# Optimization experiments

Measured on AMD Instinct MI355X. Metric: run time of the kernel, lower is better.

The kernel has to match this reference:

```python
import jax, jax.numpy as jnp
import numpy as np

GROUPS = 32
EPS = 1e-5


def setup_inputs() -> dict:
    key = jax.random.key(0)
    ks = jax.random.split(key, 8)
    B, C, H, W = 4, 512, 64, 64
    s = 1.0 / np.sqrt(C)  # conv1x1 fan-in init scale
    return {
        "x": jax.random.normal(ks[0], (B, C, H, W), dtype=jnp.float32),
        "gn_gamma": jnp.ones((C,), dtype=jnp.float32),
        "gn_beta": jnp.zeros((C,), dtype=jnp.float32),
        "wq": jax.random.normal(ks[1], (C, C), dtype=jnp.float32) * s,
        "bq": jnp.zeros((C,), dtype=jnp.float32),
        "wk": jax.random.normal(ks[2], (C, C), dtype=jnp.float32) * s,
        "bk": jnp.zeros((C,), dtype=jnp.float32),
        "wv": jax.random.normal(ks[3], (C, C), dtype=jnp.float32) * s,
        "bv": jnp.zeros((C,), dtype=jnp.float32),
    }


def reference(x, gn_gamma, gn_beta, wq, bq, wk, bk, wv, bv):
    B, C, H, W = x.shape
    N = H * W
    # GroupNorm over (channels-within-group, H, W)
    xg = x.reshape(B, GROUPS, C // GROUPS, H, W)
    mean = xg.mean(axis=(2, 3, 4), keepdims=True)
    var = xg.var(axis=(2, 3, 4), keepdims=True)
    xn = ((xg - mean) * jax.lax.rsqrt(var + EPS)).reshape(B, C, H, W)
    xn = xn * gn_gamma[None, :, None, None] + gn_beta[None, :, None, None]
    # 1x1 convs as channel matmuls over flattened spatial tokens: (B, C, N)
    xf = xn.reshape(B, C, N)
    q = jnp.einsum("oc,bcn->bon", wq, xf) + bq[None, :, None]  # (B, Co, N)
    k = jnp.einsum("oc,bcn->bon", wk, xf) + bk[None, :, None]
    v = jnp.einsum("oc,bcn->bon", wv, xf) + bv[None, :, None]
    # scores[b, m, n] = <Q_m, K_n> / sqrt(Co); full N x N matrix as in original
    scale = 1.0 / jnp.sqrt(jnp.asarray(C, dtype=x.dtype))
    scores = jnp.einsum("bcm,bcn->bmn", q, k) * scale  # (B, N, N)
    prob = jax.nn.softmax(scores, axis=-1)
    # out[b, c, m] = sum_n prob[b, m, n] * v[b, c, n]
    attn = jnp.einsum("bmn,bcn->bcm", prob, v).reshape(B, C, H, W)
    return x + attn  # ResLine is Identity since ch_in == ch_out
```

## Files before the change

### kernel.cpp

```cpp
#include <hip/hip_runtime.h>
#include <cstdint>

typedef __attribute__((ext_vector_type(8))) short short8;
typedef __attribute__((ext_vector_type(4))) float floatx4;
typedef __attribute__((ext_vector_type(8))) int intx8;

__device__ __forceinline__ unsigned short f2bf(float f) {
  unsigned int u = __float_as_uint(f);
  u += 0x7fffu + ((u >> 16) & 1u);
  return (unsigned short)(u >> 16);
}

__global__ __launch_bounds__(256) void gn_partial_kernel(
    const float* __restrict__ x, float* __restrict__ gsums) {
  const int b = blockIdx.x >> 8;
  const int g = (blockIdx.x >> 3) & 31;
  const int e = blockIdx.x & 7;
  const long long off = ((long long)(b * 512 + g * 16)) * 4096;
  const float4* xp = (const float4*)(x + off) + e * 2048;
  float s = 0.f, ss = 0.f;
  for (int i = threadIdx.x; i < 2048; i += 256) {
    float4 v = xp[i];
    s  += v.x + v.y + v.z + v.w;
    ss += v.x * v.x + v.y * v.y + v.z * v.z + v.w * v.w;
  }
  for (int off2 = 32; off2; off2 >>= 1) { s += __shfl_down(s, off2); ss += __shfl_down(ss, off2); }
  __shared__ float sb[8];
  const int lane = threadIdx.x & 63, wave = threadIdx.x >> 6;
  if (lane == 0) { sb[wave] = s; sb[4 + wave] = ss; }
  __syncthreads();
  if (threadIdx.x == 0) {
    atomicAdd(gsums + (b * 32 + g) * 2,     sb[0] + sb[1] + sb[2] + sb[3]);
    atomicAdd(gsums + (b * 32 + g) * 2 + 1, sb[4] + sb[5] + sb[6] + sb[7]);
  }
}

__global__ __launch_bounds__(256) void gn_finalize_kernel(
    const float* __restrict__ gsums, const float* __restrict__ gamma,
    const float* __restrict__ beta, float* __restrict__ scale,
    float* __restrict__ shift) {
  const int i = blockIdx.x * 256 + threadIdx.x;
  const int b = i >> 9;
  const int c = i & 511;
  const int g = c >> 4;
  const float S  = gsums[(b * 32 + g) * 2];
  const float SS = gsums[(b * 32 + g) * 2 + 1];
  const float mean = S * (1.f / 65536.f);
  const float var  = SS * (1.f / 65536.f) - mean * mean;
  const float inv  = rsqrtf(var + 1e-5f);
  const float sc = gamma[c] * inv;
  scale[i] = sc;
  shift[i] = beta[c] - mean * sc;
}

__global__ __launch_bounds__(256) void wcvt_zero_kernel(
    const float* __restrict__ wq, const float* __restrict__ wk,
    const float* __restrict__ wv, unsigned short* __restrict__ w16,
    float* __restrict__ zp, int nzero) {
  const int gi = blockIdx.x * 256 + threadIdx.x;
  if (gi < 196608) {
    const int m = gi >> 16;
    const int i = gi & 65535;
    const float* src = (m == 0) ? wq : (m == 1) ? wk : wv;
    float4 v = *((const float4*)src + i);
    ushort4 o;
    o.x = f2bf(v.x); o.y = f2bf(v.y); o.z = f2bf(v.z); o.w = f2bf(v.w);
    *((ushort4*)(w16 + (long long)m * 262144) + i) = o;
  } else {
    const int zi = gi - 196608;
    if (zi < nzero) zp[zi] = 0.f;
  }
}

__global__ __launch_bounds__(256) void norm_transpose_kernel(
    const float* __restrict__ x, const float* __restrict__ scale,
    const float* __restrict__ shift, unsigned short* __restrict__ xnt) {
  const int b = blockIdx.z;
  const int n0 = blockIdx.x * 64;
  const int c0 = blockIdx.y * 64;
  const int t = threadIdx.x;
  __shared__ unsigned short tile[64][65];
  {
    const int cl = t >> 2;
    const int nc = (t & 3) * 16;
    const int c = c0 + cl;
    const float* xp = x + ((long long)b * 512 + c) * 4096 + n0 + nc;
    const float sc = scale[b * 512 + c];
    const float sh = shift[b * 512 + c];
#pragma unroll
    for (int j = 0; j < 16; j += 4) {
      float4 v = *(const float4*)(xp + j);
      tile[cl][nc + j + 0] = f2bf(v.x * sc + sh);
      tile[cl][nc + j + 1] = f2bf(v.y * sc + sh);
      tile[cl][nc + j + 2] = f2bf(v.z * sc + sh);
      tile[cl][nc + j + 3] = f2bf(v.w * sc + sh);
    }
  }
  __syncthreads();
  {
    const int nl = t >> 2;
    const int cc = (t & 3) * 16;
    union { unsigned short u[16]; uint4 q[2]; } o;
#pragma unroll
    for (int j = 0; j < 16; ++j) o.u[j] = tile[cc + j][nl];
    unsigned short* op = xnt + ((long long)b * 4096 + n0 + nl) * 512 + c0 + cc;
    *((uint4*)op) = o.q[0];
    *((uint4*)op + 1) = o.q[1];
  }
}

__global__ __launch_bounds__(256) void zero_kernel(float* __restrict__ p, int n) {
  const int i = blockIdx.x * 256 + threadIdx.x;
  if (i < n) p[i] = 0.f;
}

template <int EPI>
__global__ __launch_bounds__(256) void gemm_tn_kernel(
    const unsigned short* __restrict__ A, const unsigned short* __restrict__ B,
    void* __restrict__ C, const float* __restrict__ bias,
    const float* __restrict__ bias2,
    int lda, int ldb, int ldc, int K,
    long long sA, long long sB, long long sC) {
  const int tid = threadIdx.x;
  const int lane = tid & 63;
  const int wave = tid >> 6;
  const int m0 = blockIdx.x * 128;
  const int n0 = blockIdx.y * 128;
  const int bz = blockIdx.z;
  A += (long long)bz * sA;
  B += (long long)bz * sB;

  __shared__ unsigned short smem[17408];
  unsigned short* As = smem;
  unsigned short* Bs = smem + 8192;

  floatx4 acc[4][4];
#pragma unroll
  for (int i = 0; i < 4; ++i)
#pragma unroll
    for (int j = 0; j < 4; ++j) acc[i][j] = (floatx4){0.f, 0.f, 0.f, 0.f};

  const unsigned short* ag[4];
  const unsigned short* bg[4];
  unsigned ldsoff[4];
#pragma unroll
  for (int i = 0; i < 4; ++i) {
    const int idx = i * 256 + tid;
    const int r = idx >> 3;
    const int g = idx & 7;
    const int gs = g ^ (r & 7);
    ag[i] = A + (long long)(m0 + r) * lda + gs * 8;
    bg[i] = B + (long long)(n0 + r) * ldb + gs * 8;
    ldsoff[i] = (unsigned)(i * 256 + wave * 64) * 8;
  }

  const int l15 = lane & 15;
  const int wm = (wave >> 1) * 64;
  const int wn = (wave & 1) * 64;

  for (int k0 = 0; k0 < K; k0 += 64) {
#pragma unroll
    for (int i = 0; i < 4; ++i) {
      __builtin_amdgcn_global_load_lds(
          (const __attribute__((address_space(1))) void*)(ag[i] + k0),
          (__attribute__((address_space(3))) void*)(As + ldsoff[i]), 16, 0, 0);
      __builtin_amdgcn_global_load_lds(
          (const __attribute__((address_space(1))) void*)(bg[i] + k0),
          (__attribute__((address_space(3))) void*)(Bs + ldsoff[i]), 16, 0, 0);
    }
    __syncthreads();
#pragma unroll
    for (int kk = 0; kk < 64; kk += 32) {
      const int gq = (kk >> 3) + (lane >> 4);
      short8 af[4], bfr[4];
#pragma unroll
      for (int mt = 0; mt < 4; ++mt) {
        const int row = wm + mt * 16 + l15;
        af[mt] = *(const short8*)&As[row * 64 + ((gq ^ (row & 7)) << 3)];
      }
#pragma unroll
      for (int nt = 0; nt < 4; ++nt) {
        const int row = wn + nt * 16 + l15;
        bfr[nt] = *(const short8*)&Bs[row * 64 + ((gq ^ (row & 7)) << 3)];
      }
#pragma unroll
      for (int mt = 0; mt < 4; ++mt)
#pragma unroll
        for (int nt = 0; nt < 4; ++nt)
          acc[mt][nt] = __builtin_amdgcn_mfma_f32_16x16x32_bf16(
              af[mt], bfr[nt], acc[mt][nt], 0, 0, 0);
    }
    __syncthreads();
  }

  const int r0 = (lane >> 4) * 4;

  if (EPI == 6) {
    unsigned char* t8 = (unsigned char*)smem;
    const float* bp = (m0 >= 512) ? bias2 : bias;
    const int mb = m0 & 511;
#pragma unroll
    for (int mt = 0; mt < 4; ++mt) {
      const int ml = wm + mt * 16 + r0;
      const float b0 = bp[mb + ml], b1 = bp[mb + ml + 1];
      const float b2 = bp[mb + ml + 2], b3 = bp[mb + ml + 3];
      const int gw = ml >> 4;
      const int mby = ml & 15;
#pragma unroll
      for (int nt = 0; nt < 4; ++nt) {
        const int nl = wn + nt * 16 + l15;
        int p = __builtin_amdgcn_cvt_pk_fp8_f32(acc[mt][nt][0] + b0,
                                                acc[mt][nt][1] + b1, 0, false);
        p = __builtin_amdgcn_cvt_pk_fp8_f32(acc[mt][nt][2] + b2,
                                            acc[mt][nt][3] + b3, p, true);
        *(int*)&t8[nl * 128 + ((gw ^ (nl & 7)) << 4) + mby] = p;
      }
    }
    __syncthreads();
    unsigned char* o8 = (unsigned char*)C + (long long)bz * sC;
#pragma unroll
    for (int t = 0; t < 4; ++t) {
      const int gid = t * 256 + tid;
      const int row = gid >> 3;
      const int gc = gid & 7;
      uint4 v = *(const uint4*)&t8[row * 128 + ((gc ^ (row & 7)) << 4)];
      *(uint4*)&o8[(long long)(n0 + row) * ldc + m0 + gc * 16] = v;
    }
    return;
  }

#pragma unroll
  for (int mt = 0; mt < 4; ++mt) {
#pragma unroll
    for (int nt = 0; nt < 4; ++nt) {
      const int nl = wn + nt * 16 + l15;
#pragma unroll
      for (int r = 0; r < 4; ++r) {
        const int ml = wm + mt * 16 + r0 + r;
        smem[ml * 136 + nl] = f2bf(acc[mt][nt][r] + bias[m0 + ml]);
      }
    }
  }
  __syncthreads();
  {
    unsigned short* o = (unsigned short*)C + (long long)bz * sC;
#pragma unroll
    for (int j = 0; j < 8; ++j) {
      const int gid = j * 256 + tid;
      const int m = gid >> 4;
      const int gc = gid & 15;
      short8 v = *(const short8*)&smem[m * 136 + gc * 8];
      *(short8*)&o[(long long)(m0 + m) * ldc + n0 + gc * 8] = v;
    }
  }
}

__global__ __launch_bounds__(256) void sgemm_fp8_kernel(
    const unsigned char* __restrict__ A, const unsigned char* __restrict__ B,
    unsigned short* __restrict__ S, float* __restrict__ lsum,
    long long sA, long long sB, long long sC, long long sL) {
  const int tid = threadIdx.x;
  const int lane = tid & 63;
  const int wave = tid >> 6;
  const int quad = lane >> 4;
  const int l15 = lane & 15;
  const int j0 = blockIdx.x * 128;
  const int i0 = blockIdx.y * 128;
  const int bz = blockIdx.z;
  A += (long long)bz * sA;
  B += (long long)bz * sB;

  __shared__ unsigned short smem[17408];
  unsigned char* As = (unsigned char*)smem;
  unsigned char* Bs = (unsigned char*)smem + 16384;

  floatx4 acc[4][4];
#pragma unroll
  for (int i = 0; i < 4; ++i)
#pragma unroll
    for (int j = 0; j < 4; ++j) acc[i][j] = (floatx4){0.f, 0.f, 0.f, 0.f};

  const unsigned char* ag[4];
  const unsigned char* bg[4];
  unsigned ldsoff[4];
#pragma unroll
  for (int i = 0; i < 4; ++i) {
    const int idx = i * 256 + tid;
    const int r = idx >> 3;
    const int g = idx & 7;
    const int gs = g ^ (r & 7);
    ag[i] = A + (long long)(j0 + r) * 1024 + gs * 16;
    bg[i] = B + (long long)(i0 + r) * 1024 + gs * 16;
    ldsoff[i] = (unsigned)(i * 256 + wave * 64) * 16;
  }

  const int wj = (wave >> 1) * 64;
  const int wi = (wave & 1) * 64;

  for (int k0 = 0; k0 < 512; k0 += 128) {
#pragma unroll
    for (int i = 0; i < 4; ++i) {
      __builtin_amdgcn_global_load_lds(
          (const __attribute__((address_space(1))) void*)(ag[i] + k0),
          (__attribute__((address_space(3))) void*)(As + ldsoff[i]), 16, 0, 0);
      __builtin_amdgcn_global_load_lds(
          (const __attribute__((address_space(1))) void*)(bg[i] + k0),
          (__attribute__((address_space(3))) void*)(Bs + ldsoff[i]), 16, 0, 0);
    }
    __syncthreads();
    intx8 af[4], bq[4];
#pragma unroll
    for (int t = 0; t < 4; ++t) {
      {
        const int row = wj + t * 16 + l15;
        const int r7 = row & 7;
        const uint4 x0 = *(const uint4*)(As + row * 128 + (((2 * quad) ^ r7) << 4));
        const uint4 x1 = *(const uint4*)(As + row * 128 + (((2 * quad + 1) ^ r7) << 4));
        af[t] = (intx8){(int)x0.x, (int)x0.y, (int)x0.z, (int)x0.w,
                        (int)x1.x, (int)x1.y, (int)x1.z, (int)x1.w};
      }
      {
        const int row = wi + t * 16 + l15;
        const int r7 = row & 7;
        const uint4 x0 = *(const uint4*)(Bs + row * 128 + (((2 * quad) ^ r7) << 4));
        const uint4 x1 = *(const uint4*)(Bs + row * 128 + (((2 * quad + 1) ^ r7) << 4));
        bq[t] = (intx8){(int)x0.x, (int)x0.y, (int)x0.z, (int)x0.w,
                        (int)x1.x, (int)x1.y, (int)x1.z, (int)x1.w};
      }
    }
#pragma unroll
    for (int jt = 0; jt < 4; ++jt)
#pragma unroll
      for (int it = 0; it < 4; ++it)
        acc[jt][it] = __builtin_amdgcn_mfma_scale_f32_16x16x128_f8f6f4(
            af[jt], bq[it], acc[jt][it], 0, 0, 0, 127, 0, 127);
    __syncthreads();
  }

  const float SCL = 0.044194173824159216f;
  const int jr = quad * 4;
  float rs_it[4] = {0.f, 0.f, 0.f, 0.f};
#pragma unroll
  for (int jt = 0; jt < 4; ++jt) {
#pragma unroll
    for (int it = 0; it < 4; ++it) {
      const int il = wi + it * 16 + l15;
      const int jl = wj + jt * 16 + jr;
      unsigned long long pk = 0;
#pragma unroll
      for (int r = 0; r < 4; ++r) {
        const float e = __expf(acc[jt][it][r] * SCL);
        rs_it[it] += e;
        pk |= (unsigned long long)(__float_as_uint(e) >> 16) << (16 * r);
      }
      *(unsigned long long*)&smem[il * 136 + jl] = pk;
    }
  }
  float* lrow = lsum + (long long)bz * sL;
#pragma unroll
  for (int it = 0; it < 4; ++it) {
    float rs = rs_it[it];
    rs += __shfl_xor(rs, 16);
    rs += __shfl_xor(rs, 32);
    if (quad == 0) atomicAdd(lrow + i0 + wi + it * 16 + l15, rs);
  }
  __syncthreads();
  unsigned short* o = S + (long long)bz * sC;
#pragma unroll
  for (int t = 0; t < 8; ++t) {
    const int gid = t * 256 + tid;
    const int row = gid >> 4;
    const int gc = gid & 15;
    short8 v = *(const short8*)&smem[row * 136 + gc * 8];
    *(short8*)&o[(long long)(i0 + row) * 4096 + j0 + gc * 8] = v;
  }
}

__device__ __forceinline__ void pv_ld_frags(
    const unsigned short* As, const unsigned short* Bs, int kk, int lane,
    int wm, int wn, short8* af, short8* bf) {
  const int l15 = lane & 15;
  const int gq = (kk >> 3) + (lane >> 4);
#pragma unroll
  for (int mt = 0; mt < 4; ++mt) {
    const int row = wm + mt * 16 + l15;
    af[mt] = *(const short8*)&As[row * 64 + ((gq ^ (row & 7)) << 3)];
  }
#pragma unroll
  for (int nt = 0; nt < 4; ++nt) {
    const int row = wn + nt * 16 + l15;
    bf[nt] = *(const short8*)&Bs[row * 64 + ((gq ^ (row & 7)) << 3)];
  }
}

__device__ __forceinline__ void pv_mfma(const short8* af, const short8* bf,
                                        floatx4 (&acc)[4][4]) {
#pragma unroll
  for (int mt = 0; mt < 4; ++mt)
#pragma unroll
    for (int nt = 0; nt < 4; ++nt)
      acc[mt][nt] = __builtin_amdgcn_mfma_f32_16x16x32_bf16(
          af[mt], bf[nt], acc[mt][nt], 0, 0, 0);
}

__global__ __launch_bounds__(512, 2) void pv_kernel(
    const unsigned short* __restrict__ A,
    const unsigned short* __restrict__ B,
    float* __restrict__ out, const float* __restrict__ res,
    const float* __restrict__ lsum,
    long long sA, long long sB, long long sC, long long sL) {
  const int id = blockIdx.x;
  const int xcd = id & 7;
  const int slot = id >> 3;
  const int m0 = (slot & 3) * 128;
  const int grp = xcd + 8 * (slot >> 2);
  const int n0 = (grp & 15) * 256;
  const int bz = grp >> 4;
  A += (long long)bz * sA;
  B += (long long)bz * sB;

  const int tid = threadIdx.x;
  const int lane = tid & 63;
  const int wave = tid >> 6;
  const int l15 = lane & 15;
  const int wm = (wave >> 2) * 64;
  const int wn = (wave & 3) * 64;

  __shared__ unsigned short smem[73728];

  floatx4 acc[4][4];
#pragma unroll
  for (int i = 0; i < 4; ++i)
#pragma unroll
    for (int j = 0; j < 4; ++j) acc[i][j] = (floatx4){0.f, 0.f, 0.f, 0.f};

  const unsigned short* ag[2];
  const unsigned short* bg[4];
  unsigned ao[2], bo[4];
#pragma unroll
  for (int j = 0; j < 2; ++j) {
    const int idx = j * 512 + tid;
    const int r = idx >> 3;
    const int g = idx & 7;
    ag[j] = A + (long long)(m0 + r) * 4096 + ((g ^ (r & 7)) << 3);
    ao[j] = (unsigned)(j * 512 + wave * 64) * 8;
  }
#pragma unroll
  for (int j = 0; j < 4; ++j) {
    const int idx = j * 512 + tid;
    const int r = idx >> 3;
    const int g = idx & 7;
    bg[j] = B + (long long)(n0 + r) * 4096 + ((g ^ (r & 7)) << 3);
    bo[j] = 8192u + (unsigned)(j * 512 + wave * 64) * 8;
  }

#define PV_GLDS(gp, lp)                                              \
  __builtin_amdgcn_global_load_lds(                                  \
      (const __attribute__((address_space(1))) void*)(gp),           \
      (__attribute__((address_space(3))) void*)(lp), 16, 0, 0)
#define PV_STA(tt, base)                                             \
  {                                                                  \
    PV_GLDS(ag[0] + (tt) * 64, smem + (base) + ao[0]);               \
    PV_GLDS(ag[1] + (tt) * 64, smem + (base) + ao[1]);               \
    PV_GLDS(bg[0] + (tt) * 64, smem + (base) + bo[0]);               \
  }
#define PV_STB(tt, base)                                             \
  {                                                                  \
    PV_GLDS(bg[1] + (tt) * 64, smem + (base) + bo[1]);               \
    PV_GLDS(bg[2] + (tt) * 64, smem + (base) + bo[2]);               \
    PV_GLDS(bg[3] + (tt) * 64, smem + (base) + bo[3]);               \
  }
#define PV_BAR()                                                     \
  {                                                                  \
    asm volatile("" ::: "memory");                                   \
    __builtin_amdgcn_s_barrier();                                    \
    asm volatile("" ::: "memory");                                   \
  }

  PV_STA(0, 0); PV_STB(0, 0);
  PV_STA(1, 24576); PV_STB(1, 24576);
  asm volatile("s_waitcnt vmcnt(6)" ::: "memory");
  PV_BAR();

  int cur = 0;
  for (int t = 0; t < 64; ++t) {
    const unsigned short* As = smem + cur * 24576;
    const unsigned short* Bs = As + 8192;
    const int nb = (cur == 0) ? 2 : cur - 1;
    const int nbase = nb * 24576;
    const bool st = (t < 62);
    short8 af[4], bf[4];

    pv_ld_frags(As, Bs, 0, lane, wm, wn, af, bf);
    if (st) PV_STA(t + 2, nbase);
    PV_BAR();
    asm volatile("s_waitcnt lgkmcnt(0)" ::: "memory");
    __builtin_amdgcn_sched_barrier(0);
    __builtin_amdgcn_s_setprio(1);
    pv_mfma(af, bf, acc);
    __builtin_amdgcn_s_setprio(0);
    PV_BAR();

    pv_ld_frags(As, Bs, 32, lane, wm, wn, af, bf);
    if (st) {
      PV_STB(t + 2, nbase);
      asm volatile("s_waitcnt vmcnt(6)" ::: "memory");
    } else {
      asm volatile("s_waitcnt vmcnt(0)" ::: "memory");
    }
    PV_BAR();
    asm volatile("s_waitcnt lgkmcnt(0)" ::: "memory");
    __builtin_amdgcn_sched_barrier(0);
    __builtin_amdgcn_s_setprio(1);
    pv_mfma(af, bf, acc);
    __builtin_amdgcn_s_setprio(0);
    PV_BAR();

    cur = (cur == 2) ? 0 : cur + 1;
  }
#undef PV_GLDS
#undef PV_STA
#undef PV_STB
#undef PV_BAR

  const int r0 = (lane >> 4) * 4;
  float* o = out + (long long)bz * sC;
  const float* rr = res + (long long)bz * sC;
  const float* lrow = lsum + (long long)bz * sL;
  float inv[4];
#pragma unroll
  for (int nt = 0; nt < 4; ++nt) inv[nt] = 1.f / lrow[n0 + wn + nt * 16 + l15];
#pragma unroll
  for (int mt = 0; mt < 4; ++mt) {
#pragma unroll
    for (int nt = 0; nt < 4; ++nt) {
      const int n = n0 + wn + nt * 16 + l15;
#pragma unroll
      for (int r = 0; r < 4; ++r) {
        const int m = m0 + wm + mt * 16 + r0 + r;
        const long long off = (long long)m * 4096 + n;
        o[off] = acc[mt][nt][r] * inv[nt] + rr[off];
      }
    }
  }
}

extern "C" void kernel_launch(void* const* d_in, const int* in_sizes, int n_in,
                              void* d_out, int out_size, void* d_ws, size_t ws_size,
                              hipStream_t stream) {
  const float* x     = (const float*)d_in[0];
  const float* gamma = (const float*)d_in[1];
  const float* beta  = (const float*)d_in[2];
  const float* wq    = (const float*)d_in[3];
  const float* bq    = (const float*)d_in[4];
  const float* wk    = (const float*)d_in[5];
  const float* bk    = (const float*)d_in[6];
  const float* wv    = (const float*)d_in[7];
  const float* bv    = (const float*)d_in[8];
  float* out = (float*)d_out;

  const long long sTok = 4096LL * 512;
  const long long sQK8 = 4096LL * 1024;
  const long long sS   = 4096LL * 4096;

  char* ws = (char*)d_ws;
  float* scale = (float*)ws;
  float* shift = (float*)(ws + 8192);
  unsigned short* w16 = (unsigned short*)(ws + 16384);
  unsigned short* xnt = (unsigned short*)(ws + 1589248);
  unsigned char*  qk8 = (unsigned char*)(ws + 18366464);
  unsigned short* vv  = (unsigned short*)(ws + 51920896);

  const bool full = ws_size >= 202982400ULL;

  float* lsum;
  int nzero;
  if (full) {
    lsum = (float*)(ws + 202915840);
    nzero = 16384 + 256;
  } else {
    lsum = (float*)(ws + 102252544);
    nzero = 4096 + 256;
  }
  float* gsums = lsum + nzero - 256;

  wcvt_zero_kernel<<<768 + (nzero + 255) / 256, 256, 0, stream>>>(
      wq, wk, wv, w16, lsum, nzero);
  gn_partial_kernel<<<1024, 256, 0, stream>>>(x, gsums);
  gn_finalize_kernel<<<8, 256, 0, stream>>>(gsums, gamma, beta, scale, shift);
  norm_transpose_kernel<<<dim3(64, 8, 4), 256, 0, stream>>>(x, scale, shift, xnt);

  gemm_tn_kernel<6><<<dim3(8, 32, 4), 256, 0, stream>>>(
      w16, xnt, qk8, bq, bk, 512, 512, 1024, 512, 0, sTok, sQK8);
  gemm_tn_kernel<2><<<dim3(4, 32, 4), 256, 0, stream>>>(
      w16 + 524288, xnt, vv, bv, nullptr, 512, 512, 4096, 512, 0, sTok, sTok);

  if (full) {
    unsigned short* S = (unsigned short*)(ws + 68698112);
    sgemm_fp8_kernel<<<dim3(32, 32, 4), 256, 0, stream>>>(
        qk8 + 512, qk8, S, lsum, sQK8, sQK8, sS, 4096);
    pv_kernel<<<256, 512, 0, stream>>>(
        vv, S, out, x, lsum, sTok, sS, sTok, 4096);
  } else {
    unsigned short* S = (unsigned short*)(ws + 68698112);
    for (int b = 0; b < 4; ++b) {
      if (b) zero_kernel<<<16, 256, 0, stream>>>(lsum, 4096);
      sgemm_fp8_kernel<<<dim3(32, 32, 1), 256, 0, stream>>>(
          qk8 + (long long)b * sQK8 + 512, qk8 + (long long)b * sQK8, S, lsum,
          0, 0, 0, 0);
      pv_kernel<<<64, 512, 0, stream>>>(
          vv + (long long)b * sTok, S, out + (long long)b * sTok,
          x + (long long)b * sTok, lsum, 0, 0, 0, 0);
    }
  }
}
```

Measured before the change: 285.6 us.

## Restructure PV kernel to 4 waves with 128x64 per-wave tiles and one barrier

The PV GEMM kernel now runs 256 threads (4 waves) per block instead of 512. Each wave owns a 128x64 output tile (8x4 MFMA accumulators) rather than 64x64. The per-k-step schedule is rewritten: both k-halves of fragments are loaded up front, one combined global-to-LDS stage is issued, and the four barriers per iteration collapse to one. The aim is to raise MFMA work per LDS fragment load and cut barrier overhead, at the cost of double the accumulator registers, fewer waves per CU to hide latency, and each thread issuing twice as many global loads.

```diff
diff --git a/kernel.cpp b/kernel.cpp
--- a/kernel.cpp
+++ b/kernel.cpp
@@ -376,34 +376,7 @@
   }
 }
 
-__device__ __forceinline__ void pv_ld_frags(
-    const unsigned short* As, const unsigned short* Bs, int kk, int lane,
-    int wm, int wn, short8* af, short8* bf) {
-  const int l15 = lane & 15;
-  const int gq = (kk >> 3) + (lane >> 4);
-#pragma unroll
-  for (int mt = 0; mt < 4; ++mt) {
-    const int row = wm + mt * 16 + l15;
-    af[mt] = *(const short8*)&As[row * 64 + ((gq ^ (row & 7)) << 3)];
-  }
-#pragma unroll
-  for (int nt = 0; nt < 4; ++nt) {
-    const int row = wn + nt * 16 + l15;
-    bf[nt] = *(const short8*)&Bs[row * 64 + ((gq ^ (row & 7)) << 3)];
-  }
-}
-
-__device__ __forceinline__ void pv_mfma(const short8* af, const short8* bf,
-                                        floatx4 (&acc)[4][4]) {
-#pragma unroll
-  for (int mt = 0; mt < 4; ++mt)
-#pragma unroll
-    for (int nt = 0; nt < 4; ++nt)
-      acc[mt][nt] = __builtin_amdgcn_mfma_f32_16x16x32_bf16(
-          af[mt], bf[nt], acc[mt][nt], 0, 0, 0);
-}
-
-__global__ __launch_bounds__(512, 2) void pv_kernel(
+__global__ __launch_bounds__(256, 1) void pv_kernel(
     const unsigned short* __restrict__ A,
     const unsigned short* __restrict__ B,
     float* __restrict__ out, const float* __restrict__ res,
@@ -423,64 +396,60 @@
   const int lane = tid & 63;
   const int wave = tid >> 6;
   const int l15 = lane & 15;
-  const int wm = (wave >> 2) * 64;
-  const int wn = (wave & 3) * 64;
+  const int wn = wave * 64;
 
   __shared__ unsigned short smem[73728];
 
-  floatx4 acc[4][4];
-#pragma unroll
-  for (int i = 0; i < 4; ++i)
+  floatx4 acc[8][4];
+#pragma unroll
+  for (int i = 0; i < 8; ++i)
 #pragma unroll
     for (int j = 0; j < 4; ++j) acc[i][j] = (floatx4){0.f, 0.f, 0.f, 0.f};
 
-  const unsigned short* ag[2];
-  const unsigned short* bg[4];
-  unsigned ao[2], bo[4];
-#pragma unroll
-  for (int j = 0; j < 2; ++j) {
-    const int idx = j * 512 + tid;
+  const unsigned short* ag[4];
+  const unsigned short* bg[8];
+  unsigned ao[4], bo[8];
+#pragma unroll
+  for (int j = 0; j < 4; ++j) {
+    const int idx = j * 256 + tid;
     const int r = idx >> 3;
     const int g = idx & 7;
     ag[j] = A + (long long)(m0 + r) * 4096 + ((g ^ (r & 7)) << 3);
-    ao[j] = (unsigned)(j * 512 + wave * 64) * 8;
-  }
-#pragma unroll
-  for (int j = 0; j < 4; ++j) {
-    const int idx = j * 512 + tid;
+    ao[j] = (unsigned)(j * 256 + wave * 64) * 8;
+  }
+#pragma unroll
+  for (int j = 0; j < 8; ++j) {
+    const int idx = j * 256 + tid;
     const int r = idx >> 3;
     const int g = idx & 7;
     bg[j] = B + (long long)(n0 + r) * 4096 + ((g ^ (r & 7)) << 3);
-    bo[j] = 8192u + (unsigned)(j * 512 + wave * 64) * 8;
+    bo[j] = 8192u + (unsigned)(j * 256 + wave * 64) * 8;
   }
 
 #define PV_GLDS(gp, lp)                                              \
   __builtin_amdgcn_global_load_lds(                                  \
       (const __attribute__((address_space(1))) void*)(gp),           \
       (__attribute__((address_space(3))) void*)(lp), 16, 0, 0)
-#define PV_STA(tt, base)                                             \
+#define PV_STAGE(tt, base)                                           \
   {                                                                  \
     PV_GLDS(ag[0] + (tt) * 64, smem + (base) + ao[0]);               \
     PV_GLDS(ag[1] + (tt) * 64, smem + (base) + ao[1]);               \
+    PV_GLDS(ag[2] + (tt) * 64, smem + (base) + ao[2]);               \
+    PV_GLDS(ag[3] + (tt) * 64, smem + (base) + ao[3]);               \
     PV_GLDS(bg[0] + (tt) * 64, smem + (base) + bo[0]);               \
-  }
-#define PV_STB(tt, base)                                             \
-  {                                                                  \
     PV_GLDS(bg[1] + (tt) * 64, smem + (base) + bo[1]);               \
     PV_GLDS(bg[2] + (tt) * 64, smem + (base) + bo[2]);               \
     PV_GLDS(bg[3] + (tt) * 64, smem + (base) + bo[3]);               \
-  }
-#define PV_BAR()                                                     \
-  {                                                                  \
-    asm volatile("" ::: "memory");                                   \
-    __builtin_amdgcn_s_barrier();                                    \
-    asm volatile("" ::: "memory");                                   \
-  }
-
-  PV_STA(0, 0); PV_STB(0, 0);
-  PV_STA(1, 24576); PV_STB(1, 24576);
-  asm volatile("s_waitcnt vmcnt(6)" ::: "memory");
-  PV_BAR();
+    PV_GLDS(bg[4] + (tt) * 64, smem + (base) + bo[4]);               \
+    PV_GLDS(bg[5] + (tt) * 64, smem + (base) + bo[5]);               \
+    PV_GLDS(bg[6] + (tt) * 64, smem + (base) + bo[6]);               \
+    PV_GLDS(bg[7] + (tt) * 64, smem + (base) + bo[7]);               \
+  }
+
+  PV_STAGE(0, 0);
+  PV_STAGE(1, 24576);
+  asm volatile("s_waitcnt vmcnt(12)" ::: "memory");
+  __builtin_amdgcn_s_barrier();
 
   int cur = 0;
   for (int t = 0; t < 64; ++t) {
@@ -489,39 +458,60 @@
     const int nb = (cur == 0) ? 2 : cur - 1;
     const int nbase = nb * 24576;
     const bool st = (t < 62);
-    short8 af[4], bf[4];
-
-    pv_ld_frags(As, Bs, 0, lane, wm, wn, af, bf);
-    if (st) PV_STA(t + 2, nbase);
-    PV_BAR();
+
+    short8 a0[8], b0[4], a1[8], b1[4];
+    const int gq0 = lane >> 4;
+    const int gq1 = 4 + (lane >> 4);
+#pragma unroll
+    for (int mt = 0; mt < 8; ++mt) {
+      const int row = mt * 16 + l15;
+      a0[mt] = *(const short8*)&As[row * 64 + ((gq0 ^ (row & 7)) << 3)];
+    }
+#pragma unroll
+    for (int nt = 0; nt < 4; ++nt) {
+      const int row = wn + nt * 16 + l15;
+      b0[nt] = *(const short8*)&Bs[row * 64 + ((gq0 ^ (row & 7)) << 3)];
+    }
+    __builtin_amdgcn_sched_barrier(0);
+#pragma unroll
+    for (int mt = 0; mt < 8; ++mt) {
+      const int row = mt * 16 + l15;
+      a1[mt] = *(const short8*)&As[row * 64 + ((gq1 ^ (row & 7)) << 3)];
+    }
+#pragma unroll
+    for (int nt = 0; nt < 4; ++nt) {
+      const int row = wn + nt * 16 + l15;
+      b1[nt] = *(const short8*)&Bs[row * 64 + ((gq1 ^ (row & 7)) << 3)];
+    }
+    __builtin_amdgcn_sched_barrier(0);
+    if (st) PV_STAGE(t + 2, nbase);
+    asm volatile("s_waitcnt lgkmcnt(12)" ::: "memory");
+    __builtin_amdgcn_sched_barrier(0);
+#pragma unroll
+    for (int mt = 0; mt < 8; ++mt)
+#pragma unroll
+      for (int nt = 0; nt < 4; ++nt)
+        acc[mt][nt] = __builtin_amdgcn_mfma_f32_16x16x32_bf16(
+            a0[mt], b0[nt], acc[mt][nt], 0, 0, 0);
     asm volatile("s_waitcnt lgkmcnt(0)" ::: "memory");
     __builtin_amdgcn_sched_barrier(0);
-    __builtin_amdgcn_s_setprio(1);
-    pv_mfma(af, bf, acc);
-    __builtin_amdgcn_s_setprio(0);
-    PV_BAR();
-
-    pv_ld_frags(As, Bs, 32, lane, wm, wn, af, bf);
+#pragma unroll
+    for (int mt = 0; mt < 8; ++mt)
+#pragma unroll
+      for (int nt = 0; nt < 4; ++nt)
+        acc[mt][nt] = __builtin_amdgcn_mfma_f32_16x16x32_bf16(
+            a1[mt], b1[nt], acc[mt][nt], 0, 0, 0);
     if (st) {
-      PV_STB(t + 2, nbase);
-      asm volatile("s_waitcnt vmcnt(6)" ::: "memory");
+      asm volatile("s_waitcnt vmcnt(12)" ::: "memory");
     } else {
       asm volatile("s_waitcnt vmcnt(0)" ::: "memory");
     }
-    PV_BAR();
-    asm volatile("s_waitcnt lgkmcnt(0)" ::: "memory");
-    __builtin_amdgcn_sched_barrier(0);
-    __builtin_amdgcn_s_setprio(1);
-    pv_mfma(af, bf, acc);
-    __builtin_amdgcn_s_setprio(0);
-    PV_BAR();
+    __builtin_amdgcn_s_barrier();
 
     cur = (cur == 2) ? 0 : cur + 1;
   }
 #undef PV_GLDS
-#undef PV_STA
-#undef PV_STB
-#undef PV_BAR
+#undef PV_STAGE
 
   const int r0 = (lane >> 4) * 4;
   float* o = out + (long long)bz * sC;
@@ -531,13 +521,13 @@
 #pragma unroll
   for (int nt = 0; nt < 4; ++nt) inv[nt] = 1.f / lrow[n0 + wn + nt * 16 + l15];
 #pragma unroll
-  for (int mt = 0; mt < 4; ++mt) {
+  for (int mt = 0; mt < 8; ++mt) {
 #pragma unroll
     for (int nt = 0; nt < 4; ++nt) {
       const int n = n0 + wn + nt * 16 + l15;
 #pragma unroll
       for (int r = 0; r < 4; ++r) {
-        const int m = m0 + wm + mt * 16 + r0 + r;
+        const int m = m0 + mt * 16 + r0 + r;
         const long long off = (long long)m * 4096 + n;
         o[off] = acc[mt][nt][r] * inv[nt] + rr[off];
       }
@@ -599,7 +589,7 @@
     unsigned short* S = (unsigned short*)(ws + 68698112);
     sgemm_fp8_kernel<<<dim3(32, 32, 4), 256, 0, stream>>>(
         qk8 + 512, qk8, S, lsum, sQK8, sQK8, sS, 4096);
-    pv_kernel<<<256, 512, 0, stream>>>(
+    pv_kernel<<<256, 256, 0, stream>>>(
         vv, S, out, x, lsum, sTok, sS, sTok, 4096);
   } else {
     unsigned short* S = (unsigned short*)(ws + 68698112);
@@ -608,7 +598,7 @@
       sgemm_fp8_kernel<<<dim3(32, 32, 1), 256, 0, stream>>>(
           qk8 + (long long)b * sQK8 + 512, qk8 + (long long)b * sQK8, S, lsum,
           0, 0, 0, 0);
-      pv_kernel<<<64, 512, 0, stream>>>(
+      pv_kernel<<<64, 256, 0, stream>>>(
           vv + (long long)b * sTok, S, out + (long long)b * sTok,
           x + (long long)b * sTok, lsum, 0, 0, 0, 0);
     }
```

Measured after the change: 285.7 us. Within noise of the previous version (+0.0%).

## Store exp scores and V in FP8 and run PV GEMM with FP8 MFMA

Applied to the files above, without the earlier changes.

The softmax numerators in the score kernel are now written as FP8 instead of BF16, and the V projection epilogue emits FP8 in the row-major layout. The PV kernel is rewritten to use the 16x16x128 scaled FP8 MFMA with 128-byte K tiles, halving the K loop trip count and the number of barriers per tile. This halves the bytes of the large score matrix written and read, at the cost of lower precision in probabilities and V values.

```diff
diff --git a/kernel.cpp b/kernel.cpp
--- a/kernel.cpp
+++ b/kernel.cpp
@@ -229,6 +229,39 @@
     return;
   }
 
+  if (EPI == 3) {
+    unsigned char* t8 = (unsigned char*)smem;
+#pragma unroll
+    for (int mt = 0; mt < 4; ++mt) {
+      const int ml = wm + mt * 16 + r0;
+      const float b0 = bias[m0 + ml],     b1 = bias[m0 + ml + 1];
+      const float b2 = bias[m0 + ml + 2], b3 = bias[m0 + ml + 3];
+#pragma unroll
+      for (int nt = 0; nt < 4; ++nt) {
+        const int nl = wn + nt * 16 + l15;
+        int p0 = __builtin_amdgcn_cvt_pk_fp8_f32(acc[mt][nt][0] + b0,
+                                                 acc[mt][nt][1] + b1, 0, false);
+        int p1 = __builtin_amdgcn_cvt_pk_fp8_f32(acc[mt][nt][2] + b2,
+                                                 acc[mt][nt][3] + b3, 0, false);
+        t8[(ml + 0) * 144 + nl] = (unsigned char)(p0 & 0xff);
+        t8[(ml + 1) * 144 + nl] = (unsigned char)((p0 >> 8) & 0xff);
+        t8[(ml + 2) * 144 + nl] = (unsigned char)(p1 & 0xff);
+        t8[(ml + 3) * 144 + nl] = (unsigned char)((p1 >> 8) & 0xff);
+      }
+    }
+    __syncthreads();
+    unsigned char* o8 = (unsigned char*)C + (long long)bz * sC;
+#pragma unroll
+    for (int t = 0; t < 4; ++t) {
+      const int gid = t * 256 + tid;
+      const int row = gid >> 3;
+      const int gc = gid & 7;
+      uint4 v = *(const uint4*)&t8[row * 144 + gc * 16];
+      *(uint4*)&o8[(long long)(m0 + row) * ldc + n0 + gc * 16] = v;
+    }
+    return;
+  }
+
 #pragma unroll
   for (int mt = 0; mt < 4; ++mt) {
 #pragma unroll
@@ -257,7 +290,7 @@
 
 __global__ __launch_bounds__(256) void sgemm_fp8_kernel(
     const unsigned char* __restrict__ A, const unsigned char* __restrict__ B,
-    unsigned short* __restrict__ S, float* __restrict__ lsum,
+    unsigned char* __restrict__ S, float* __restrict__ lsum,
     long long sA, long long sB, long long sC, long long sL) {
   const int tid = threadIdx.x;
   const int lane = tid & 63;
@@ -339,6 +372,7 @@
 
   const float SCL = 0.044194173824159216f;
   const int jr = quad * 4;
+  unsigned char* t8 = (unsigned char*)smem;
   float rs_it[4] = {0.f, 0.f, 0.f, 0.f};
 #pragma unroll
   for (int jt = 0; jt < 4; ++jt) {
@@ -346,14 +380,14 @@
     for (int it = 0; it < 4; ++it) {
       const int il = wi + it * 16 + l15;
       const int jl = wj + jt * 16 + jr;
-      unsigned long long pk = 0;
-#pragma unroll
-      for (int r = 0; r < 4; ++r) {
-        const float e = __expf(acc[jt][it][r] * SCL);
-        rs_it[it] += e;
-        pk |= (unsigned long long)(__float_as_uint(e) >> 16) << (16 * r);
-      }
-      *(unsigned long long*)&smem[il * 136 + jl] = pk;
+      const float e0 = __expf(acc[jt][it][0] * SCL);
+      const float e1 = __expf(acc[jt][it][1] * SCL);
+      const float e2 = __expf(acc[jt][it][2] * SCL);
+      const float e3 = __expf(acc[jt][it][3] * SCL);
+      rs_it[it] += e0 + e1 + e2 + e3;
+      int p = __builtin_amdgcn_cvt_pk_fp8_f32(e0, e1, 0, false);
+      p = __builtin_amdgcn_cvt_pk_fp8_f32(e2, e3, p, true);
+      *(int*)&t8[il * 144 + jl] = p;
     }
   }
   float* lrow = lsum + (long long)bz * sL;
@@ -365,47 +399,20 @@
     if (quad == 0) atomicAdd(lrow + i0 + wi + it * 16 + l15, rs);
   }
   __syncthreads();
-  unsigned short* o = S + (long long)bz * sC;
-#pragma unroll
-  for (int t = 0; t < 8; ++t) {
+  unsigned char* o = S + (long long)bz * sC;
+#pragma unroll
+  for (int t = 0; t < 4; ++t) {
     const int gid = t * 256 + tid;
-    const int row = gid >> 4;
-    const int gc = gid & 15;
-    short8 v = *(const short8*)&smem[row * 136 + gc * 8];
-    *(short8*)&o[(long long)(i0 + row) * 4096 + j0 + gc * 8] = v;
-  }
-}
-
-__device__ __forceinline__ void pv_ld_frags(
-    const unsigned short* As, const unsigned short* Bs, int kk, int lane,
-    int wm, int wn, short8* af, short8* bf) {
-  const int l15 = lane & 15;
-  const int gq = (kk >> 3) + (lane >> 4);
-#pragma unroll
-  for (int mt = 0; mt < 4; ++mt) {
-    const int row = wm + mt * 16 + l15;
-    af[mt] = *(const short8*)&As[row * 64 + ((gq ^ (row & 7)) << 3)];
-  }
-#pragma unroll
-  for (int nt = 0; nt < 4; ++nt) {
-    const int row = wn + nt * 16 + l15;
-    bf[nt] = *(const short8*)&Bs[row * 64 + ((gq ^ (row & 7)) << 3)];
-  }
-}
-
-__device__ __forceinline__ void pv_mfma(const short8* af, const short8* bf,
-                                        floatx4 (&acc)[4][4]) {
-#pragma unroll
-  for (int mt = 0; mt < 4; ++mt)
-#pragma unroll
-    for (int nt = 0; nt < 4; ++nt)
-      acc[mt][nt] = __builtin_amdgcn_mfma_f32_16x16x32_bf16(
-          af[mt], bf[nt], acc[mt][nt], 0, 0, 0);
+    const int row = gid >> 3;
+    const int gc = gid & 7;
+    uint4 v = *(const uint4*)&t8[row * 144 + gc * 16];
+    *(uint4*)&o[(long long)(i0 + row) * 4096 + j0 + gc * 16] = v;
+  }
 }
 
 __global__ __launch_bounds__(512, 2) void pv_kernel(
-    const unsigned short* __restrict__ A,
-    const unsigned short* __restrict__ B,
+    const unsigned char* __restrict__ A,
+    const unsigned char* __restrict__ B,
     float* __restrict__ out, const float* __restrict__ res,
     const float* __restrict__ lsum,
     long long sA, long long sB, long long sC, long long sL) {
@@ -423,10 +430,11 @@
   const int lane = tid & 63;
   const int wave = tid >> 6;
   const int l15 = lane & 15;
+  const int quad = lane >> 4;
   const int wm = (wave >> 2) * 64;
   const int wn = (wave & 3) * 64;
 
-  __shared__ unsigned short smem[73728];
+  __shared__ unsigned char smem[147456];
 
   floatx4 acc[4][4];
 #pragma unroll
@@ -434,94 +442,96 @@
 #pragma unroll
     for (int j = 0; j < 4; ++j) acc[i][j] = (floatx4){0.f, 0.f, 0.f, 0.f};
 
-  const unsigned short* ag[2];
-  const unsigned short* bg[4];
+  const unsigned char* ag[2];
+  const unsigned char* bg[4];
   unsigned ao[2], bo[4];
 #pragma unroll
   for (int j = 0; j < 2; ++j) {
     const int idx = j * 512 + tid;
     const int r = idx >> 3;
     const int g = idx & 7;
-    ag[j] = A + (long long)(m0 + r) * 4096 + ((g ^ (r & 7)) << 3);
-    ao[j] = (unsigned)(j * 512 + wave * 64) * 8;
+    ag[j] = A + (long long)(m0 + r) * 4096 + ((g ^ (r & 7)) << 4);
+    ao[j] = (unsigned)(j * 512 + wave * 64) * 16;
   }
 #pragma unroll
   for (int j = 0; j < 4; ++j) {
     const int idx = j * 512 + tid;
     const int r = idx >> 3;
     const int g = idx & 7;
-    bg[j] = B + (long long)(n0 + r) * 4096 + ((g ^ (r & 7)) << 3);
-    bo[j] = 8192u + (unsigned)(j * 512 + wave * 64) * 8;
+    bg[j] = B + (long long)(n0 + r) * 4096 + ((g ^ (r & 7)) << 4);
+    bo[j] = 16384u + (unsigned)(j * 512 + wave * 64) * 16;
   }
 
 #define PV_GLDS(gp, lp)                                              \
   __builtin_amdgcn_global_load_lds(                                  \
       (const __attribute__((address_space(1))) void*)(gp),           \
       (__attribute__((address_space(3))) void*)(lp), 16, 0, 0)
-#define PV_STA(tt, base)                                             \
+#define PV_STAGE(tt, base)                                           \
   {                                                                  \
-    PV_GLDS(ag[0] + (tt) * 64, smem + (base) + ao[0]);               \
-    PV_GLDS(ag[1] + (tt) * 64, smem + (base) + ao[1]);               \
-    PV_GLDS(bg[0] + (tt) * 64, smem + (base) + bo[0]);               \
-  }
-#define PV_STB(tt, base)                                             \
-  {                                                                  \
-    PV_GLDS(bg[1] + (tt) * 64, smem + (base) + bo[1]);               \
-    PV_GLDS(bg[2] + (tt) * 64, smem + (base) + bo[2]);               \
-    PV_GLDS(bg[3] + (tt) * 64, smem + (base) + bo[3]);               \
-  }
-#define PV_BAR()                                                     \
-  {                                                                  \
-    asm volatile("" ::: "memory");                                   \
-    __builtin_amdgcn_s_barrier();                                    \
-    asm volatile("" ::: "memory");                                   \
-  }
-
-  PV_STA(0, 0); PV_STB(0, 0);
-  PV_STA(1, 24576); PV_STB(1, 24576);
+    PV_GLDS(ag[0] + (tt) * 128, smem + (base) + ao[0]);              \
+    PV_GLDS(ag[1] + (tt) * 128, smem + (base) + ao[1]);              \
+    PV_GLDS(bg[0] + (tt) * 128, smem + (base) + bo[0]);              \
+    PV_GLDS(bg[1] + (tt) * 128, smem + (base) + bo[1]);              \
+    PV_GLDS(bg[2] + (tt) * 128, smem + (base) + bo[2]);              \
+    PV_GLDS(bg[3] + (tt) * 128, smem + (base) + bo[3]);              \
+  }
+
+  PV_STAGE(0, 0);
+  PV_STAGE(1, 49152);
   asm volatile("s_waitcnt vmcnt(6)" ::: "memory");
-  PV_BAR();
+  __builtin_amdgcn_s_barrier();
 
   int cur = 0;
-  for (int t = 0; t < 64; ++t) {
-    const unsigned short* As = smem + cur * 24576;
-    const unsigned short* Bs = As + 8192;
+  for (int t = 0; t < 32; ++t) {
+    const unsigned char* As = smem + cur * 49152;
+    const unsigned char* Bs = As + 16384;
     const int nb = (cur == 0) ? 2 : cur - 1;
-    const int nbase = nb * 24576;
-    const bool st = (t < 62);
-    short8 af[4], bf[4];
-
-    pv_ld_frags(As, Bs, 0, lane, wm, wn, af, bf);
-    if (st) PV_STA(t + 2, nbase);
-    PV_BAR();
+    const int nbase = nb * 49152;
+    const bool st = (t < 30);
+
+    intx8 af[4], bq[4];
+#pragma unroll
+    for (int tt = 0; tt < 4; ++tt) {
+      {
+        const int row = wm + tt * 16 + l15;
+        const int r7 = row & 7;
+        const uint4 x0 = *(const uint4*)(As + row * 128 + (((2 * quad) ^ r7) << 4));
+        const uint4 x1 = *(const uint4*)(As + row * 128 + (((2 * quad + 1) ^ r7) << 4));
+        af[tt] = (intx8){(int)x0.x, (int)x0.y, (int)x0.z, (int)x0.w,
+                         (int)x1.x, (int)x1.y, (int)x1.z, (int)x1.w};
+      }
+      {
+        const int row = wn + tt * 16 + l15;
+        const int r7 = row & 7;
+        const uint4 x0 = *(const uint4*)(Bs + row * 128 + (((2 * quad) ^ r7) << 4));
+        const uint4 x1 = *(const uint4*)(Bs + row * 128 + (((2 * quad + 1) ^ r7) << 4));
+        bq[tt] = (intx8){(int)x0.x, (int)x0.y, (int)x0.z, (int)x0.w,
+                         (int)x1.x, (int)x1.y, (int)x1.z, (int)x1.w};
+      }
+    }
+    __builtin_amdgcn_sched_barrier(0);
+    if (st) PV_STAGE(t + 2, nbase);
     asm volatile("s_waitcnt lgkmcnt(0)" ::: "memory");
     __builtin_amdgcn_sched_barrier(0);
     __builtin_amdgcn_s_setprio(1);
-    pv_mfma(af, bf, acc);
+#pragma unroll
+    for (int mt = 0; mt < 4; ++mt)
+#pragma unroll
+      for (int nt = 0; nt < 4; ++nt)
+        acc[mt][nt] = __builtin_amdgcn_mfma_scale_f32_16x16x128_f8f6f4(
+            af[mt], bq[nt], acc[mt][nt], 0, 0, 0, 127, 0, 127);
     __builtin_amdgcn_s_setprio(0);
-    PV_BAR();
-
-    pv_ld_frags(As, Bs, 32, lane, wm, wn, af, bf);
     if (st) {
-      PV_STB(t + 2, nbase);
       asm volatile("s_waitcnt vmcnt(6)" ::: "memory");
     } else {
       asm volatile("s_waitcnt vmcnt(0)" ::: "memory");
     }
-    PV_BAR();
-    asm volatile("s_waitcnt lgkmcnt(0)" ::: "memory");
-    __builtin_amdgcn_sched_barrier(0);
-    __builtin_amdgcn_s_setprio(1);
-    pv_mfma(af, bf, acc);
-    __builtin_amdgcn_s_setprio(0);
-    PV_BAR();
+    __builtin_amdgcn_s_barrier();
 
     cur = (cur == 2) ? 0 : cur + 1;
   }
 #undef PV_GLDS
-#undef PV_STA
-#undef PV_STB
-#undef PV_BAR
+#undef PV_STAGE
 
   const int r0 = (lane >> 4) * 4;
   float* o = out + (long long)bz * sC;
@@ -561,7 +571,8 @@
 
   const long long sTok = 4096LL * 512;
   const long long sQK8 = 4096LL * 1024;
-  const long long sS   = 4096LL * 4096;
+  const long long sS8  = 4096LL * 4096;
+  const long long sV8  = 512LL * 4096;
 
   char* ws = (char*)d_ws;
   float* scale = (float*)ws;
@@ -569,7 +580,7 @@
   unsigned short* w16 = (unsigned short*)(ws + 16384);
   unsigned short* xnt = (unsigned short*)(ws + 1589248);
   unsigned char*  qk8 = (unsigned char*)(ws + 18366464);
-  unsigned short* vv  = (unsigned short*)(ws + 51920896);
+  unsigned char*  vv8 = (unsigned char*)(ws + 51920896);
 
   const bool full = ws_size >= 202982400ULL;
 
@@ -592,24 +603,24 @@
 
   gemm_tn_kernel<6><<<dim3(8, 32, 4), 256, 0, stream>>>(
       w16, xnt, qk8, bq, bk, 512, 512, 1024, 512, 0, sTok, sQK8);
-  gemm_tn_kernel<2><<<dim3(4, 32, 4), 256, 0, stream>>>(
-      w16 + 524288, xnt, vv, bv, nullptr, 512, 512, 4096, 512, 0, sTok, sTok);
+  gemm_tn_kernel<3><<<dim3(4, 32, 4), 256, 0, stream>>>(
+      w16 + 524288, xnt, vv8, bv, nullptr, 512, 512, 4096, 512, 0, sTok, sV8);
 
   if (full) {
-    unsigned short* S = (unsigned short*)(ws + 68698112);
+    unsigned char* S8 = (unsigned char*)(ws + 68698112);
     sgemm_fp8_kernel<<<dim3(32, 32, 4), 256, 0, stream>>>(
-        qk8 + 512, qk8, S, lsum, sQK8, sQK8, sS, 4096);
+        qk8 + 512, qk8, S8, lsum, sQK8, sQK8, sS8, 4096);
     pv_kernel<<<256, 512, 0, stream>>>(
-        vv, S, out, x, lsum, sTok, sS, sTok, 4096);
+        vv8, S8, out, x, lsum, sV8, sS8, sTok, 4096);
   } else {
-    unsigned short* S = (unsigned short*)(ws + 68698112);
+    unsigned char* S8 = (unsigned char*)(ws + 68698112);
     for (int b = 0; b < 4; ++b) {
       if (b) zero_kernel<<<16, 256, 0, stream>>>(lsum, 4096);
       sgemm_fp8_kernel<<<dim3(32, 32, 1), 256, 0, stream>>>(
-          qk8 + (long long)b * sQK8 + 512, qk8 + (long long)b * sQK8, S, lsum,
+          qk8 + (long long)b * sQK8 + 512, qk8 + (long long)b * sQK8, S8, lsum,
           0, 0, 0, 0);
       pv_kernel<<<64, 512, 0, stream>>>(
-          vv + (long long)b * sTok, S, out + (long long)b * sTok,
+          vv8 + (long long)b * sV8, S8, out + (long long)b * sTok,
           x + (long long)b * sTok, lsum, 0, 0, 0, 0);
     }
   }
```

Result: faster. 242.9 us (-14.9%).
